# Performance work log

Hardware: AMD Instinct MI355X
Metric: run time of the kernel (lower is better)

Reference implementation:

```python
import jax, jax.numpy as jnp
import numpy as np

N_NODES = 100000


def setup_inputs() -> dict:
    key = jax.random.key(0)
    k_x, k_src, k_dst, k_w = jax.random.split(key, 4)
    X = jax.random.normal(k_x, (N_NODES, 128), dtype=jnp.float32)
    src = jax.random.randint(k_src, (3200000,), 0, N_NODES, dtype=jnp.int64)
    dst = jax.random.randint(k_dst, (3200000,), 0, N_NODES, dtype=jnp.int64)
    # Linear(2*in_channels=256 -> out_channels=128); kaiming-ish scale
    W = jax.random.normal(k_w, (256, 128), dtype=jnp.float32) * (1.0 / np.sqrt(256.0))
    b = jnp.zeros((128,), dtype=jnp.float32)
    return {"X": X, "src": src, "dst": dst, "W": W, "b": b}


def reference(X, src, dst, W, b):
    # G.v2v(X, aggr='mean'): scatter-mean of neighbor features over edges
    msg = X[src]                                              # [E, d] gather
    summed = jax.ops.segment_sum(msg, dst, num_segments=N_NODES)  # [N, d]
    deg = jax.ops.segment_sum(jnp.ones_like(dst, dtype=X.dtype), dst,
                              num_segments=N_NODES)           # [N]
    X_nbr = summed / jnp.maximum(deg, 1.0)[:, None]           # mean, safe for deg=0
    # concat self + neighbor mean, linear, relu (dropout is eval-mode no-op)
    H = jnp.concatenate([X, X_nbr], axis=1)                   # [N, 2d]
    out = jax.nn.relu(H @ W + b)                              # [N, out]
    return out
```

## Files before the change

kernel.cpp:

```cpp
#include <hip/hip_runtime.h>
#include <cstddef>
#include <cstdint>


#define NODES_PER_BLOCK 32
#define PART_SHIFT 8
#define PART_SZ 256
#define MAXP 448
#define CHUNK 4096
#define CAPP 8704
#define CAPN 96

typedef __attribute__((ext_vector_type(8))) short bf16x8;
typedef __attribute__((ext_vector_type(4))) float f32x4;

__device__ __forceinline__ int clampi(int v, int hi) {
    v = v < 0 ? 0 : v;
    return v >= hi ? hi - 1 : v;
}

__device__ __forceinline__ unsigned short bf16_rne(float f) {
    unsigned int u = __float_as_uint(f);
    unsigned int r = (u + 0x7FFFu + ((u >> 16) & 1u)) >> 16;
    return (unsigned short)r;
}

__device__ __forceinline__ unsigned pack2(float a, float b) {
    return (unsigned)bf16_rne(a) | ((unsigned)bf16_rne(b) << 16);
}

__device__ __forceinline__ void acc_bf16x8(float* a, uint4 r) {
    a[0] += __uint_as_float(r.x << 16);
    a[1] += __uint_as_float(r.x & 0xFFFF0000u);
    a[2] += __uint_as_float(r.y << 16);
    a[3] += __uint_as_float(r.y & 0xFFFF0000u);
    a[4] += __uint_as_float(r.z << 16);
    a[5] += __uint_as_float(r.z & 0xFFFF0000u);
    a[6] += __uint_as_float(r.w << 16);
    a[7] += __uint_as_float(r.w & 0xFFFF0000u);
}

__device__ __forceinline__ int wave_excl_scan64(int v, int lane) {
    int x = v;
#pragma unroll
    for (int off = 1; off < 64; off <<= 1) {
        int y = __shfl_up(x, off, 64);
        if (lane >= off) x += y;
    }
    return x - v;
}

__device__ void do_xw_block(int xb,
    const float* __restrict__ X, unsigned short* __restrict__ Xb, int total4,
    const float* __restrict__ W, unsigned short* __restrict__ Wswz)
{
    int i = xb * 256 + threadIdx.x;
    if (i < 256 * 128) {
        int k = i >> 7, n = i & 127;
        int kk = k >> 5, q = (k >> 3) & 3, j = k & 7;
        int cg = n >> 4, nn = n & 15;
        int lane = q * 16 + nn;
        Wswz[((size_t)(kk * 8 + cg) * 64 + lane) * 8 + j] =
            bf16_rne(W[(size_t)k * 128 + n]);
    }
    if (i < total4) {
        float4 v = *(const float4*)(X + (size_t)i * 4);
        ushort4 o;
        o.x = bf16_rne(v.x); o.y = bf16_rne(v.y);
        o.z = bf16_rne(v.z); o.w = bf16_rne(v.w);
        *(ushort4*)(Xb + (size_t)i * 4) = o;
    }
}

__global__ __launch_bounds__(256) void hist_convert(
    const int* __restrict__ dst, int* __restrict__ counts,
    int E, int N, int P, int nChunk,
    const float* __restrict__ X, unsigned short* __restrict__ Xb, int total4,
    const float* __restrict__ W, unsigned short* __restrict__ Wswz)
{
    const int bid = (int)blockIdx.x;
    if (bid >= nChunk) {
        do_xw_block(bid - nChunk, X, Xb, total4, W, Wswz);
        return;
    }
    __shared__ int hist[MAXP];
    const int tid = threadIdx.x;
    const int c0  = bid * CHUNK;
    const int cnt = (E - c0 < CHUNK) ? (E - c0) : CHUNK;

    for (int i = tid; i < P; i += 256) hist[i] = 0;
    __syncthreads();

#pragma unroll
    for (int g = 0; g < 4; ++g) {
        int i0 = (g * 256 + tid) * 4;
        if (i0 + 4 <= cnt) {
            int4 d4 = *(const int4*)(dst + c0 + i0);
            atomicAdd(&hist[clampi(d4.x, N) >> PART_SHIFT], 1);
            atomicAdd(&hist[clampi(d4.y, N) >> PART_SHIFT], 1);
            atomicAdd(&hist[clampi(d4.z, N) >> PART_SHIFT], 1);
            atomicAdd(&hist[clampi(d4.w, N) >> PART_SHIFT], 1);
        } else {
            for (int i = i0; i < cnt && i < i0 + 4; ++i)
                atomicAdd(&hist[clampi(dst[c0 + i], N) >> PART_SHIFT], 1);
        }
    }
    __syncthreads();
    for (int i = tid; i < P; i += 256)
        counts[(size_t)i * nChunk + bid] = hist[i];
}

__global__ __launch_bounds__(64) void scan_bases(
    int* __restrict__ counts, int* __restrict__ pcnt, int nChunk)
{
    const int p    = (int)blockIdx.x;
    const int lane = (int)threadIdx.x;
    int* row = counts + (size_t)p * nChunk;
    int carry = 0;
    for (int j = 0; j < nChunk; j += 64) {
        int idx = j + lane;
        int v = (idx < nChunk) ? row[idx] : 0;
        int ex = wave_excl_scan64(v, lane);
        if (idx < nChunk) row[idx] = carry + ex;
        carry += __shfl(ex + v, 63, 64);
    }
    if (lane == 0) pcnt[p] = carry;
}

__global__ __launch_bounds__(256) void scatter_parts(
    const int* __restrict__ src, const int* __restrict__ dst,
    const int* __restrict__ counts, unsigned long long* __restrict__ parts,
    int E, int N, int P, int nChunk, int capp)
{
    __shared__ unsigned long long sbuf[CHUNK];
    __shared__ int hist[MAXP], base_s[MAXP], gbase[MAXP];
    const int bid = (int)blockIdx.x;
    const int tid = threadIdx.x;
    const int c0  = bid * CHUNK;
    const int cnt = (E - c0 < CHUNK) ? (E - c0) : CHUNK;

    for (int i = tid; i < P; i += 256) {
        hist[i] = 0;
        gbase[i] = counts[(size_t)i * nChunk + bid];
    }
    __syncthreads();

    int s[16], d[16], r[16];
#pragma unroll
    for (int g = 0; g < 4; ++g) {
        int i0 = (g * 256 + tid) * 4;
        if (i0 + 4 <= cnt) {
            int4 d4 = *(const int4*)(dst + c0 + i0);
            int4 s4 = *(const int4*)(src + c0 + i0);
            d[g * 4 + 0] = clampi(d4.x, N); s[g * 4 + 0] = clampi(s4.x, N);
            d[g * 4 + 1] = clampi(d4.y, N); s[g * 4 + 1] = clampi(s4.y, N);
            d[g * 4 + 2] = clampi(d4.z, N); s[g * 4 + 2] = clampi(s4.z, N);
            d[g * 4 + 3] = clampi(d4.w, N); s[g * 4 + 3] = clampi(s4.w, N);
        } else {
#pragma unroll
            for (int k = 0; k < 4; ++k) {
                int i = i0 + k;
                if (i < cnt) {
                    d[g * 4 + k] = clampi(dst[c0 + i], N);
                    s[g * 4 + k] = clampi(src[c0 + i], N);
                } else {
                    d[g * 4 + k] = -1; s[g * 4 + k] = 0;
                }
            }
        }
    }
#pragma unroll
    for (int k = 0; k < 16; ++k)
        r[k] = (d[k] >= 0) ? atomicAdd(&hist[d[k] >> PART_SHIFT], 1) : 0;
    __syncthreads();

    if (tid < 64) {
        int pref[7]; int run = 0;
#pragma unroll
        for (int k2 = 0; k2 < 7; ++k2) {
            int idx = tid * 7 + k2;
            int v = (idx < P) ? hist[idx] : 0;
            pref[k2] = run; run += v;
        }
        int lx = wave_excl_scan64(run, tid);
#pragma unroll
        for (int k2 = 0; k2 < 7; ++k2) {
            int idx = tid * 7 + k2;
            if (idx < P) base_s[idx] = pref[k2] + lx;
        }
    }
    __syncthreads();

#pragma unroll
    for (int k = 0; k < 16; ++k) {
        if (d[k] >= 0) {
            int p = d[k] >> PART_SHIFT;
            sbuf[base_s[p] + r[k]] =
                ((unsigned long long)(unsigned)d[k] << 32) | (unsigned)s[k];
        }
    }
    __syncthreads();

    for (int i = tid; i < cnt; i += 256) {
        unsigned long long rec = sbuf[i];
        int p = ((int)(rec >> 32)) >> PART_SHIFT;
        int slot = gbase[p] + (i - base_s[p]);
        if (slot < capp) parts[(size_t)p * capp + slot] = rec;
    }
}

__global__ __launch_bounds__(256) void gather_gemm(
    const unsigned short* __restrict__ Xb,
    const unsigned long long* __restrict__ parts,
    const int* __restrict__ pcnt,
    int capp,
    const unsigned short* __restrict__ Wswz,
    const float* __restrict__ bias,
    float* __restrict__ out, int N, int nwg)
{
    __shared__ unsigned short Hb[NODES_PER_BLOCK][256];
    __shared__ int lsrc[NODES_PER_BLOCK][CAPN];
    __shared__ int ldeg[NODES_PER_BLOCK];
    const int tid = threadIdx.x;

    const int bid  = (int)blockIdx.x;
    const int q8   = nwg >> 3;
    const int work = (bid & 7) * q8 + (bid >> 3);
    const int p    = work >> 3;
    const int g    = work & 7;
    const int n0   = p * PART_SZ + g * NODES_PER_BLOCK;
    if (n0 >= N) return;

    if (tid < NODES_PER_BLOCK) ldeg[tid] = 0;
    __syncthreads();

    {
        int cnt = pcnt[p]; if (cnt > capp) cnt = capp;
        const unsigned long long* prec = parts + (size_t)p * capp;
        int i = tid;
        for (; i + 256 < cnt; i += 512) {
            unsigned long long r0 = prec[i];
            unsigned long long r1 = prec[i + 256];
            int dl0 = ((int)(r0 >> 32)) & (PART_SZ - 1);
            int dl1 = ((int)(r1 >> 32)) & (PART_SZ - 1);
            if ((dl0 >> 5) == g) {
                int r = atomicAdd(&ldeg[dl0 & 31], 1);
                if (r < CAPN) lsrc[dl0 & 31][r] = (int)(r0 & 0xFFFFFFFFu);
            }
            if ((dl1 >> 5) == g) {
                int r = atomicAdd(&ldeg[dl1 & 31], 1);
                if (r < CAPN) lsrc[dl1 & 31][r] = (int)(r1 & 0xFFFFFFFFu);
            }
        }
        for (; i < cnt; i += 256) {
            unsigned long long r0 = prec[i];
            int dl0 = ((int)(r0 >> 32)) & (PART_SZ - 1);
            if ((dl0 >> 5) == g) {
                int r = atomicAdd(&ldeg[dl0 & 31], 1);
                if (r < CAPN) lsrc[dl0 & 31][r] = (int)(r0 & 0xFFFFFFFFu);
            }
        }
    }
    __syncthreads();

    {
        const int sub = tid & 15;
        const int grp = tid >> 4;
        const int f0  = sub * 8;
        for (int ii = 0; ii < 2; ++ii) {
            const int v = grp * 2 + ii;
            const int n = n0 + v;
            if (n >= N) continue;
            const int dg  = ldeg[v];
            const int dgl = dg < CAPN ? dg : CAPN;
            const int* brow = lsrc[v];
            float acc[8] = {0.f, 0.f, 0.f, 0.f, 0.f, 0.f, 0.f, 0.f};
            int t = 0;
            for (; t + 8 <= dgl; t += 8) {
                int i0 = brow[t],     i1 = brow[t + 1];
                int i2 = brow[t + 2], i3 = brow[t + 3];
                int i4 = brow[t + 4], i5 = brow[t + 5];
                int i6 = brow[t + 6], i7 = brow[t + 7];
                uint4 r0 = *(const uint4*)(Xb + (size_t)i0 * 128 + f0);
                uint4 r1 = *(const uint4*)(Xb + (size_t)i1 * 128 + f0);
                uint4 r2 = *(const uint4*)(Xb + (size_t)i2 * 128 + f0);
                uint4 r3 = *(const uint4*)(Xb + (size_t)i3 * 128 + f0);
                uint4 r4 = *(const uint4*)(Xb + (size_t)i4 * 128 + f0);
                uint4 r5 = *(const uint4*)(Xb + (size_t)i5 * 128 + f0);
                uint4 r6 = *(const uint4*)(Xb + (size_t)i6 * 128 + f0);
                uint4 r7 = *(const uint4*)(Xb + (size_t)i7 * 128 + f0);
                acc_bf16x8(acc, r0); acc_bf16x8(acc, r1);
                acc_bf16x8(acc, r2); acc_bf16x8(acc, r3);
                acc_bf16x8(acc, r4); acc_bf16x8(acc, r5);
                acc_bf16x8(acc, r6); acc_bf16x8(acc, r7);
            }
            for (; t + 4 <= dgl; t += 4) {
                int i0 = brow[t],     i1 = brow[t + 1];
                int i2 = brow[t + 2], i3 = brow[t + 3];
                uint4 r0 = *(const uint4*)(Xb + (size_t)i0 * 128 + f0);
                uint4 r1 = *(const uint4*)(Xb + (size_t)i1 * 128 + f0);
                uint4 r2 = *(const uint4*)(Xb + (size_t)i2 * 128 + f0);
                uint4 r3 = *(const uint4*)(Xb + (size_t)i3 * 128 + f0);
                acc_bf16x8(acc, r0); acc_bf16x8(acc, r1);
                acc_bf16x8(acc, r2); acc_bf16x8(acc, r3);
            }
            for (; t < dgl; ++t) {
                uint4 r0 = *(const uint4*)(Xb + (size_t)brow[t] * 128 + f0);
                acc_bf16x8(acc, r0);
            }
            const float inv = 1.0f / fmaxf((float)dg, 1.0f);
            *(uint4*)&Hb[v][f0] = *(const uint4*)(Xb + (size_t)n * 128 + f0);
            uint4 mo;
            mo.x = pack2(acc[0] * inv, acc[1] * inv);
            mo.y = pack2(acc[2] * inv, acc[3] * inv);
            mo.z = pack2(acc[4] * inv, acc[5] * inv);
            mo.w = pack2(acc[6] * inv, acc[7] * inv);
            *(uint4*)&Hb[v][128 + f0] = mo;
        }
    }
    __syncthreads();

    const int lane = tid & 63;
    const int wave = tid >> 6;
    const int tile = wave >> 1;
    const int wv2  = wave & 1;
    const int m    = lane & 15;
    const int quad = lane >> 4;
    f32x4 acc0 = {0.f, 0.f, 0.f, 0.f};
    f32x4 acc1 = {0.f, 0.f, 0.f, 0.f};
    f32x4 acc2 = {0.f, 0.f, 0.f, 0.f};
    f32x4 acc3 = {0.f, 0.f, 0.f, 0.f};
#pragma unroll
    for (int kk = 0; kk < 8; ++kk) {
        bf16x8 a = *(const bf16x8*)&Hb[tile * 16 + m][kk * 32 + quad * 8];
        const unsigned short* wp =
            Wswz + ((size_t)(kk * 8 + wv2 * 4) * 64 + lane) * 8;
        bf16x8 b0 = *(const bf16x8*)(wp);
        bf16x8 b1 = *(const bf16x8*)(wp + 64 * 8);
        bf16x8 b2 = *(const bf16x8*)(wp + 2 * 64 * 8);
        bf16x8 b3 = *(const bf16x8*)(wp + 3 * 64 * 8);
        acc0 = __builtin_amdgcn_mfma_f32_16x16x32_bf16(a, b0, acc0, 0, 0, 0);
        acc1 = __builtin_amdgcn_mfma_f32_16x16x32_bf16(a, b1, acc1, 0, 0, 0);
        acc2 = __builtin_amdgcn_mfma_f32_16x16x32_bf16(a, b2, acc2, 0, 0, 0);
        acc3 = __builtin_amdgcn_mfma_f32_16x16x32_bf16(a, b3, acc3, 0, 0, 0);
    }
    f32x4 accs[4] = {acc0, acc1, acc2, acc3};
#pragma unroll
    for (int c = 0; c < 4; ++c) {
        int feat = wv2 * 64 + c * 16 + m;
        float bv = bias[feat];
#pragma unroll
        for (int r = 0; r < 4; ++r) {
            int node = n0 + tile * 16 + quad * 4 + r;
            if (node < N)
                out[(size_t)node * 128 + feat] = fmaxf(accs[c][r] + bv, 0.f);
        }
    }
}

static inline size_t align256(size_t x) { return (x + 255) & ~(size_t)255; }

extern "C" void kernel_launch(void* const* d_in, const int* in_sizes, int n_in,
                              void* d_out, int out_size, void* d_ws, size_t ws_size,
                              hipStream_t stream) {
    const float* X    = (const float*)d_in[0];
    const int*   src  = (const int*)d_in[1];
    const int*   dst  = (const int*)d_in[2];
    const float* W    = (const float*)d_in[3];
    const float* bias = (const float*)d_in[4];
    float* out = (float*)d_out;

    const int N = in_sizes[0] / 128;
    const int E = in_sizes[1];
    const int P = (N + PART_SZ - 1) >> PART_SHIFT;
    const int nChunk = (E + CHUNK - 1) / CHUNK;

    char* base = (char*)d_ws;
    size_t o_pcnt   = 0;
    size_t o_counts = align256((size_t)P * 4);
    size_t o_wswz   = o_counts + align256((size_t)P * nChunk * 4);
    size_t o_xb     = o_wswz   + align256((size_t)256 * 128 * 2);
    size_t o_parts  = o_xb     + align256((size_t)N * 128 * 2);

    int capp = CAPP;
    {
        size_t avail = (ws_size > o_parts) ? (ws_size - o_parts) : 0;
        size_t fit = avail / ((size_t)P * 8);
        if (fit < (size_t)capp) capp = (int)fit;
    }

    int* pcnt                 = (int*)(base + o_pcnt);
    int* counts               = (int*)(base + o_counts);
    unsigned short* Wswz      = (unsigned short*)(base + o_wswz);
    unsigned short* Xb        = (unsigned short*)(base + o_xb);
    unsigned long long* parts = (unsigned long long*)(base + o_parts);

    const int total4 = (N * 128) / 4;
    const int nXw    = (total4 + 255) / 256;
    const int nwg    = P * 8;

    hist_convert<<<nChunk + nXw, 256, 0, stream>>>(
        dst, counts, E, N, P, nChunk, X, Xb, total4, W, Wswz);
    scan_bases<<<P, 64, 0, stream>>>(counts, pcnt, nChunk);
    scatter_parts<<<nChunk, 256, 0, stream>>>(
        src, dst, counts, parts, E, N, P, nChunk, capp);
    gather_gemm<<<nwg, 256, 0, stream>>>(
        Xb, parts, pcnt, capp, Wswz, bias, out, N, nwg);
}
```

Baseline: 290.4 us.

## Pack partition records to 32 bits and widen gather_gemm blocks to 64 nodes

Edge records in the partition buffer are packed as 32-bit words (8-bit local dst, 24-bit src) instead of 64-bit pairs, which halves scatter writes and the partition reads in gather_gemm. gather_gemm now handles 64 nodes per block with 512 threads, so each partition is scanned by 4 blocks rather than 8, cutting the redundant rereads of partition records. The counts matrix is transposed to chunk-major, which makes the hist and scatter accesses coalesced but the scan strided. The risks are the smaller per-node cap (CAPN 80) and node indices limited to 24 bits.

```diff
diff --git a/kernel.cpp b/kernel.cpp
--- a/kernel.cpp
+++ b/kernel.cpp
@@ -3,13 +3,13 @@
 #include <cstdint>
 
 
-#define NODES_PER_BLOCK 32
+#define NODES_PER_BLOCK 64
 #define PART_SHIFT 8
 #define PART_SZ 256
 #define MAXP 448
 #define CHUNK 4096
 #define CAPP 8704
-#define CAPN 96
+#define CAPN 80
 
 typedef __attribute__((ext_vector_type(8))) short bf16x8;
 typedef __attribute__((ext_vector_type(4))) float f32x4;
@@ -107,21 +107,20 @@
     }
     __syncthreads();
     for (int i = tid; i < P; i += 256)
-        counts[(size_t)i * nChunk + bid] = hist[i];
+        counts[(size_t)bid * P + i] = hist[i];
 }
 
 __global__ __launch_bounds__(64) void scan_bases(
-    int* __restrict__ counts, int* __restrict__ pcnt, int nChunk)
+    int* __restrict__ counts, int* __restrict__ pcnt, int P, int nChunk)
 {
     const int p    = (int)blockIdx.x;
     const int lane = (int)threadIdx.x;
-    int* row = counts + (size_t)p * nChunk;
     int carry = 0;
     for (int j = 0; j < nChunk; j += 64) {
         int idx = j + lane;
-        int v = (idx < nChunk) ? row[idx] : 0;
+        int v = (idx < nChunk) ? counts[(size_t)idx * P + p] : 0;
         int ex = wave_excl_scan64(v, lane);
-        if (idx < nChunk) row[idx] = carry + ex;
+        if (idx < nChunk) counts[(size_t)idx * P + p] = carry + ex;
         carry += __shfl(ex + v, 63, 64);
     }
     if (lane == 0) pcnt[p] = carry;
@@ -129,10 +128,11 @@
 
 __global__ __launch_bounds__(256) void scatter_parts(
     const int* __restrict__ src, const int* __restrict__ dst,
-    const int* __restrict__ counts, unsigned long long* __restrict__ parts,
+    const int* __restrict__ counts, unsigned int* __restrict__ parts,
     int E, int N, int P, int nChunk, int capp)
 {
-    __shared__ unsigned long long sbuf[CHUNK];
+    __shared__ unsigned int sbuf[CHUNK];
+    __shared__ unsigned short pbuf[CHUNK];
     __shared__ int hist[MAXP], base_s[MAXP], gbase[MAXP];
     const int bid = (int)blockIdx.x;
     const int tid = threadIdx.x;
@@ -141,7 +141,7 @@
 
     for (int i = tid; i < P; i += 256) {
         hist[i] = 0;
-        gbase[i] = counts[(size_t)i * nChunk + bid];
+        gbase[i] = counts[(size_t)bid * P + i];
     }
     __syncthreads();
 
@@ -195,28 +195,29 @@
     for (int k = 0; k < 16; ++k) {
         if (d[k] >= 0) {
             int p = d[k] >> PART_SHIFT;
-            sbuf[base_s[p] + r[k]] =
-                ((unsigned long long)(unsigned)d[k] << 32) | (unsigned)s[k];
+            int pos = base_s[p] + r[k];
+            sbuf[pos] = ((unsigned)(d[k] & (PART_SZ - 1)) << 24) |
+                        (unsigned)s[k];
+            pbuf[pos] = (unsigned short)p;
         }
     }
     __syncthreads();
 
     for (int i = tid; i < cnt; i += 256) {
-        unsigned long long rec = sbuf[i];
-        int p = ((int)(rec >> 32)) >> PART_SHIFT;
+        int p = pbuf[i];
         int slot = gbase[p] + (i - base_s[p]);
-        if (slot < capp) parts[(size_t)p * capp + slot] = rec;
-    }
-}
-
-__global__ __launch_bounds__(256) void gather_gemm(
+        if (slot < capp) parts[(size_t)p * capp + slot] = sbuf[i];
+    }
+}
+
+__global__ __launch_bounds__(512) void gather_gemm(
     const unsigned short* __restrict__ Xb,
-    const unsigned long long* __restrict__ parts,
+    const unsigned int* __restrict__ parts,
     const int* __restrict__ pcnt,
     int capp,
     const unsigned short* __restrict__ Wswz,
     const float* __restrict__ bias,
-    float* __restrict__ out, int N, int nwg)
+    float* __restrict__ out, int N, int P, int nwgp)
 {
     __shared__ unsigned short Hb[NODES_PER_BLOCK][256];
     __shared__ int lsrc[NODES_PER_BLOCK][CAPN];
@@ -224,10 +225,11 @@
     const int tid = threadIdx.x;
 
     const int bid  = (int)blockIdx.x;
-    const int q8   = nwg >> 3;
+    const int q8   = nwgp >> 3;
     const int work = (bid & 7) * q8 + (bid >> 3);
-    const int p    = work >> 3;
-    const int g    = work & 7;
+    if (work >= P * 4) return;
+    const int p    = work >> 2;
+    const int g    = work & 3;
     const int n0   = p * PART_SZ + g * NODES_PER_BLOCK;
     if (n0 >= N) return;
 
@@ -236,28 +238,28 @@
 
     {
         int cnt = pcnt[p]; if (cnt > capp) cnt = capp;
-        const unsigned long long* prec = parts + (size_t)p * capp;
+        const unsigned int* prec = parts + (size_t)p * capp;
         int i = tid;
-        for (; i + 256 < cnt; i += 512) {
-            unsigned long long r0 = prec[i];
-            unsigned long long r1 = prec[i + 256];
-            int dl0 = ((int)(r0 >> 32)) & (PART_SZ - 1);
-            int dl1 = ((int)(r1 >> 32)) & (PART_SZ - 1);
-            if ((dl0 >> 5) == g) {
-                int r = atomicAdd(&ldeg[dl0 & 31], 1);
-                if (r < CAPN) lsrc[dl0 & 31][r] = (int)(r0 & 0xFFFFFFFFu);
-            }
-            if ((dl1 >> 5) == g) {
-                int r = atomicAdd(&ldeg[dl1 & 31], 1);
-                if (r < CAPN) lsrc[dl1 & 31][r] = (int)(r1 & 0xFFFFFFFFu);
-            }
-        }
-        for (; i < cnt; i += 256) {
-            unsigned long long r0 = prec[i];
-            int dl0 = ((int)(r0 >> 32)) & (PART_SZ - 1);
-            if ((dl0 >> 5) == g) {
-                int r = atomicAdd(&ldeg[dl0 & 31], 1);
-                if (r < CAPN) lsrc[dl0 & 31][r] = (int)(r0 & 0xFFFFFFFFu);
+        for (; i + 512 < cnt; i += 1024) {
+            unsigned int r0 = prec[i];
+            unsigned int r1 = prec[i + 512];
+            int dl0 = (int)(r0 >> 24);
+            int dl1 = (int)(r1 >> 24);
+            if ((dl0 >> 6) == g) {
+                int r = atomicAdd(&ldeg[dl0 & 63], 1);
+                if (r < CAPN) lsrc[dl0 & 63][r] = (int)(r0 & 0xFFFFFFu);
+            }
+            if ((dl1 >> 6) == g) {
+                int r = atomicAdd(&ldeg[dl1 & 63], 1);
+                if (r < CAPN) lsrc[dl1 & 63][r] = (int)(r1 & 0xFFFFFFu);
+            }
+        }
+        for (; i < cnt; i += 512) {
+            unsigned int r0 = prec[i];
+            int dl0 = (int)(r0 >> 24);
+            if ((dl0 >> 6) == g) {
+                int r = atomicAdd(&ldeg[dl0 & 63], 1);
+                if (r < CAPN) lsrc[dl0 & 63][r] = (int)(r0 & 0xFFFFFFu);
             }
         }
     }
@@ -378,32 +380,32 @@
     char* base = (char*)d_ws;
     size_t o_pcnt   = 0;
     size_t o_counts = align256((size_t)P * 4);
-    size_t o_wswz   = o_counts + align256((size_t)P * nChunk * 4);
+    size_t o_wswz   = o_counts + align256((size_t)nChunk * P * 4);
     size_t o_xb     = o_wswz   + align256((size_t)256 * 128 * 2);
     size_t o_parts  = o_xb     + align256((size_t)N * 128 * 2);
 
     int capp = CAPP;
     {
         size_t avail = (ws_size > o_parts) ? (ws_size - o_parts) : 0;
-        size_t fit = avail / ((size_t)P * 8);
+        size_t fit = avail / ((size_t)P * 4);
         if (fit < (size_t)capp) capp = (int)fit;
     }
 
-    int* pcnt                 = (int*)(base + o_pcnt);
-    int* counts               = (int*)(base + o_counts);
-    unsigned short* Wswz      = (unsigned short*)(base + o_wswz);
-    unsigned short* Xb        = (unsigned short*)(base + o_xb);
-    unsigned long long* parts = (unsigned long long*)(base + o_parts);
+    int* pcnt            = (int*)(base + o_pcnt);
+    int* counts          = (int*)(base + o_counts);
+    unsigned short* Wswz = (unsigned short*)(base + o_wswz);
+    unsigned short* Xb   = (unsigned short*)(base + o_xb);
+    unsigned int* parts  = (unsigned int*)(base + o_parts);
 
     const int total4 = (N * 128) / 4;
     const int nXw    = (total4 + 255) / 256;
-    const int nwg    = P * 8;
+    const int nwgp   = ((P * 4 + 7) / 8) * 8;
 
     hist_convert<<<nChunk + nXw, 256, 0, stream>>>(
         dst, counts, E, N, P, nChunk, X, Xb, total4, W, Wswz);
-    scan_bases<<<P, 64, 0, stream>>>(counts, pcnt, nChunk);
+    scan_bases<<<P, 64, 0, stream>>>(counts, pcnt, P, nChunk);
     scatter_parts<<<nChunk, 256, 0, stream>>>(
         src, dst, counts, parts, E, N, P, nChunk, capp);
-    gather_gemm<<<nwg, 256, 0, stream>>>(
-        Xb, parts, pcnt, capp, Wswz, bias, out, N, nwg);
-}
+    gather_gemm<<<nwgp, 512, 0, stream>>>(
+        Xb, parts, pcnt, capp, Wswz, bias, out, N, P, nwgp);
+}
```

Result: faster. 280.2 us (-3.5%).
